# Kernel tuning notes

Hardware: AMD Instinct MI355X
Metric: run time of the kernel (lower is better)

## Reference

```python
import jax, jax.numpy as jnp
import numpy as np
from jax.scipy.special import logsumexp

NEG = -1e9  # surrogate for -inf (keeps masking arithmetic and grads NaN-free)
ABSTRACT_PEN = 0.5


def setup_inputs() -> dict:
    key = jax.random.key(0)
    ks = jax.random.split(key, 5)
    B, T, b = 32, 256, 16
    action_logps = jax.nn.log_softmax(jax.random.normal(ks[0], (B, T, b)), axis=-1)
    stop_logps = jax.nn.log_softmax(jax.random.normal(ks[1], (B, T + 1, b, 2)), axis=-1)
    start_logps = jax.nn.log_softmax(jax.random.normal(ks[2], (B, T + 1, b)), axis=-1)
    causal_pens = jax.random.uniform(ks[3], (B, T + 1, T + 1, b))
    lengths = jax.random.randint(ks[4], (B,), 1, T + 1)
    masks = (jnp.arange(T)[None, :] < lengths[:, None]).astype(jnp.float32)
    return {"action_logps": action_logps, "stop_logps": stop_logps,
            "start_logps": start_logps, "causal_pens": causal_pens,
            "masks": masks, "lengths": lengths}


def _cc_loss(action_logps, stop_logps, start_logps, causal_pens, masks, lengths):
    B, T, b = action_logps.shape
    start_logps = start_logps - ABSTRACT_PEN
    stop_logps = stop_logps[..., ::-1]  # STOP_IX == 0 -> flip so index 1 = stop

    a_ts = jnp.swapaxes(action_logps, 0, 1)            # [T,B,b]
    stop_ts = jnp.swapaxes(stop_logps[:, 1:], 0, 1)    # [T,B,b,2]  stop_logps[:, t+1]
    start_ts = jnp.swapaxes(start_logps[:, :T], 0, 1)  # [T,B,b]
    m_ts = jnp.swapaxes(masks, 0, 1)                   # [T,B]

    # ---- cc_fw: f[t] has shape [B,b,t,2]; pad segment-start axis to T ----
    f0 = jnp.full((B, b, T, 2), NEG).at[:, 0, 0, 1].set(0.0)

    def fw_step(f_prev, xs):
        a_t, stop_t, start_t, t = xs
        # continue current option: positions < t-1
        cont = f_prev[..., 0:1] + a_t[:, :, None, None] + stop_t[:, :, None, :]
        # start a new option at position t-1
        seg = logsumexp(f_prev[..., 1], axis=(1, 2))  # [B]
        new_seg = seg[:, None, None] + start_t[:, :, None] + a_t[:, :, None] + stop_t  # [B,b,2]
        idx = jnp.arange(T)[None, None, :, None]
        f_t = jnp.where(idx == t - 1, new_seg[:, :, None, :], cont)
        return f_t, f_t

    _, F = jax.lax.scan(fw_step, f0, (a_ts, stop_ts, start_ts, jnp.arange(1, T + 1)))
    F_full = jnp.concatenate([f0[None], F], axis=0)  # [T+1,B,b,T,2]
    total_logp = logsumexp(F_full[lengths, jnp.arange(B)][..., 1], axis=(1, 2))  # [B]

    # ---- cc_bw ----
    fT = jnp.full((B, b, 2), NEG).at[:, :, 1].set(0.0)

    def bw_step(f_next, xs):
        a_t, stop_t, start_t, m_t = xs
        f0c = a_t + logsumexp(stop_t + f_next, axis=2)  # [B,b]
        f1c = logsumexp(start_t[:, :, None] + a_t[:, :, None] + stop_t + f_next, axis=(1, 2))  # [B]
        f_t = jnp.stack([f0c, jnp.broadcast_to(f1c[:, None], f0c.shape)], axis=-1)
        done = jnp.stack([jnp.full_like(f0c, NEG), jnp.zeros_like(f0c)], axis=-1)
        f_t = jnp.where(m_t[:, None, None] > 0, f_t, done)
        return f_t, f_t

    _, BW = jax.lax.scan(bw_step, fT, (a_ts, stop_ts, start_ts, m_ts), reverse=True)
    BW_full = jnp.concatenate([BW, fT[None]], axis=0)  # [T+1,B,b,2]

    # ---- causal-consistency penalty expectation ----
    # marginal[t-1, B, b, start] = fw f[t][...,1] + bw f[t][...,1]
    marg = F[..., 1] + BW_full[1:][..., 1][:, :, :, None]          # [T,B,b,T]
    probs = jnp.exp(marg - total_logp[None, :, None, None])        # padded starts -> 0
    # pen[t-1, B, b, start] = causal_pens[B, start, t, b]
    pen = jnp.transpose(causal_pens[:, :T, 1:, :], (2, 0, 3, 1))   # [T,B,b,T]
    total_cc = jnp.sum(jnp.sum(probs * pen, axis=(2, 3)) * m_ts)
    return jnp.stack([jnp.sum(total_logp), total_cc])


def reference(action_logps, stop_logps, start_logps, causal_pens, masks, lengths):
    return _cc_loss(action_logps, stop_logps, start_logps, causal_pens, masks, lengths)
```

## Files before the change

kernel.cpp:

```cpp
#include <hip/hip_runtime.h>

constexpr int B  = 32;
constexpr int T  = 256;
constexpr int NB = 16;
#define NEGV   (-1000000000.0f)
#define INVLN2 1.4426950408889634f
#define LN2    0.6931471805599453f
#define AP2    (0.5f * 1.4426950408889634f)

__device__ __forceinline__ float fexp2(float x) { return exp2f(x); }
__device__ __forceinline__ float flog2(float x) { return __log2f(x); }

template<int C>
__device__ __forceinline__ float dppmv(float x) {
    return __int_as_float(__builtin_amdgcn_update_dpp(
        0, __float_as_int(x), C, 0xF, 0xF, true));
}

__device__ __forceinline__ float lse16_2(float y) {
    float m = y;
    m = fmaxf(m, dppmv<0xB1>(m));
    m = fmaxf(m, dppmv<0x4E>(m));
    m = fmaxf(m, dppmv<0x141>(m));
    m = fmaxf(m, dppmv<0x140>(m));
    float s = fexp2(y - m);
    s += dppmv<0xB1>(s);
    s += dppmv<0x4E>(s);
    s += dppmv<0x141>(s);
    s += dppmv<0x140>(s);
    return m + flog2(s);
}

__device__ __forceinline__ float lse2_2(float a, float b) {
    float m = fmaxf(a, b);
    return m + flog2(fexp2(a - m) + fexp2(b - m));
}

__global__ __launch_bounds__(256) void scan_kernel(
    const float* __restrict__ act_g,
    const float* __restrict__ stp_g,
    const float* __restrict__ str_g,
    const int*   __restrict__ len_g,
    float* __restrict__ Wbuf,
    float* __restrict__ TLbuf,
    float* __restrict__ Ubuf,
    float* __restrict__ Vbuf)
{
    __shared__ float sm[16384];
    float* act  = sm;
    float* stp  = sm + 4096;
    float* strt = sm + 4096 + 8192;

    const int beta = blockIdx.x;
    const int tid  = threadIdx.x;

    {
        const float4* a4 = (const float4*)(act_g + (size_t)beta * (T * NB));
        const float4* s4 = (const float4*)(stp_g + (size_t)beta * ((T + 1) * NB * 2) + 32);
        const float4* t4 = (const float4*)(str_g + (size_t)beta * ((T + 1) * NB));
        float4* actv = (float4*)act;
        float4* stpv = (float4*)stp;
        float4* strv = (float4*)strt;
        for (int i = tid; i < 1024; i += 256) {
            float4 v = a4[i];
            actv[i] = make_float4(v.x*INVLN2, v.y*INVLN2, v.z*INVLN2, v.w*INVLN2);
        }
        for (int i = tid; i < 2048; i += 256) {
            float4 v = s4[i];
            stpv[i] = make_float4(v.x*INVLN2, v.y*INVLN2, v.z*INVLN2, v.w*INVLN2);
        }
        for (int i = tid; i < 1024; i += 256) {
            float4 v = t4[i];
            strv[i] = make_float4(v.x*INVLN2, v.y*INVLN2, v.z*INVLN2, v.w*INVLN2);
        }
    }
    __syncthreads();

    const int wid  = tid >> 6;
    const int lane = tid & 63;
    const int b    = lane & 15;
    const int L    = len_g[beta];

    if (wid == 0) {
        float* Ub = Ubuf + (size_t)beta * (T * NB);
        float* Vb = Vbuf + (size_t)beta * ((T + 1) * NB);
        float PA = 0.f, Q = 0.f;
        float R = strt[b] - AP2;
        if (lane < 16) Ub[b] = R;
        float TL = 0.f;

        float  ca  = act[b];
        float2 cs  = *(const float2*)(stp + b * 2);
        float  cst = strt[16 + b];

        for (int t = 1; t <= T; ++t) {
            float  na  = act[(t & 255) * 16 + b];
            float2 ns  = *(const float2*)(stp + (t & 255) * 32 + b * 2);
            float  nst = strt[((t + 1) & 255) * 16 + b];

            PA += ca;
            float V = PA + Q + cs.x;
            float G = lse16_2(R + V);
            if (t == L) TL = G;
            Q += cs.y;
            if (lane < 16) Vb[t * 16 + b] = V;
            if (t < T) {
                float U = G + (cst - AP2) - PA - Q;
                if (lane < 16) Ub[t * 16 + b] = U;
                R = lse2_2(R, U);
            }
            ca = na; cs = ns; cst = nst;
        }
        if (lane == 0) TLbuf[beta] = TL;
    } else if (wid == 1) {
        float fn0 = NEGV, fn1 = 0.f;
        if (lane == 0) Wbuf[beta * (T + 1) + T] = 0.f;

        float  ca  = act[(T - 1) * 16 + b];
        float2 cs  = *(const float2*)(stp + (T - 1) * 32 + b * 2);
        float  cst = strt[(T - 1) * 16 + b];

        for (int i = T - 1; i >= 0; --i) {
            const int pr = (i - 1) & 255;
            float  na  = act[pr * 16 + b];
            float2 ns  = *(const float2*)(stp + pr * 32 + b * 2);
            float  nst = strt[pr * 16 + b];

            float t0  = cs.y + fn0;
            float t1  = cs.x + fn1;
            float f0c = ca + lse2_2(t0, t1);
            float f1c = lse16_2((cst - AP2) + f0c);
            const bool mk = (i < L);
            fn0 = mk ? f0c : NEGV;
            fn1 = mk ? f1c : 0.f;
            if (i >= 1 && lane == 0) Wbuf[beta * (T + 1) + i] = fn1;
            ca = na; cs = ns; cst = nst;
        }
    }
}

__global__ __launch_bounds__(256) void cc_kernel(
    const float* __restrict__ pens,
    const int*   __restrict__ len_g,
    const float* __restrict__ Wbuf,
    const float* __restrict__ TLbuf,
    const float* __restrict__ Ubuf,
    const float* __restrict__ Vbuf,
    float* __restrict__ part)
{
    const int beta = blockIdx.x;
    const int t    = blockIdx.y + 1;
    const int tid  = threadIdx.x;
    const int pidx = blockIdx.y * B + beta;
    const int L    = len_g[beta];
    if (t > L) { if (tid == 0) part[pidx] = 0.f; return; }

    const float c0 = Wbuf[beta * (T + 1) + t] - TLbuf[beta];
    const float4* U4 = (const float4*)(Ubuf + (size_t)beta * (T * NB));
    const float4* P4 = (const float4*)(pens + (size_t)beta * ((size_t)(T+1)*(T+1)*NB)
                                            + (size_t)t * NB);
    const int q = tid & 3;
    float4 vq = ((const float4*)(Vbuf + (size_t)beta * ((T + 1) * NB) + t * NB))[q];
    vq.x += c0; vq.y += c0; vq.z += c0; vq.w += c0;

    float local = 0.f;
    const int n4 = t * 4;
    for (int i4 = tid; i4 < n4; i4 += 256) {
        const int tau = i4 >> 2;
        float4 u = U4[i4];
        float4 p = P4[(size_t)tau * ((T + 1) * 4) + (i4 & 3)];
        local += fexp2(u.x + vq.x) * p.x + fexp2(u.y + vq.y) * p.y
               + fexp2(u.z + vq.z) * p.z + fexp2(u.w + vq.w) * p.w;
    }
#pragma unroll
    for (int off = 1; off < 64; off <<= 1) local += __shfl_xor(local, off);
    __shared__ float red[4];
    if ((tid & 63) == 0) red[tid >> 6] = local;
    __syncthreads();
    if (tid == 0) part[pidx] = red[0] + red[1] + red[2] + red[3];
}

__global__ __launch_bounds__(256) void final_kernel(
    const float* __restrict__ part, const float* __restrict__ TLbuf,
    float* __restrict__ out)
{
    const int tid = threadIdx.x;
    const float4* p4 = (const float4*)part;
    float s = 0.f;
#pragma unroll
    for (int k = 0; k < 8; ++k) {
        float4 v = p4[tid + 256 * k];
        s += v.x + v.y + v.z + v.w;
    }
#pragma unroll
    for (int off = 1; off < 64; off <<= 1) s += __shfl_xor(s, off);
    __shared__ float red[4];
    if ((tid & 63) == 0) red[tid >> 6] = s;
    __syncthreads();
    if (tid == 0) out[1] = red[0] + red[1] + red[2] + red[3];

    float tl = (tid < 32) ? TLbuf[tid] : 0.f;
    if (tid < 64) {
#pragma unroll
        for (int off = 1; off < 32; off <<= 1) tl += __shfl_xor(tl, off);
        if (tid == 0) out[0] = tl * LN2;
    }
}

extern "C" void kernel_launch(void* const* d_in, const int* in_sizes, int n_in,
                              void* d_out, int out_size, void* d_ws, size_t ws_size,
                              hipStream_t stream) {
    (void)in_sizes; (void)n_in; (void)out_size; (void)ws_size;
    const float* act  = (const float*)d_in[0];
    const float* stp  = (const float*)d_in[1];
    const float* strt = (const float*)d_in[2];
    const float* pens = (const float*)d_in[3];
    const int*   lens = (const int*)d_in[5];
    float* out = (float*)d_out;

    float* ws    = (float*)d_ws;
    float* Wbuf  = ws;
    float* TLbuf = Wbuf + B * (T + 1);
    float* Ubuf  = TLbuf + B;
    float* Vbuf  = Ubuf + (size_t)B * T * NB;
    float* part  = Vbuf + (size_t)B * (T+1) * NB;

    scan_kernel<<<B, 256, 0, stream>>>(act, stp, strt, lens, Wbuf, TLbuf, Ubuf, Vbuf);
    cc_kernel<<<dim3(B, T), 256, 0, stream>>>(pens, lens, Wbuf, TLbuf, Ubuf, Vbuf, part);
    final_kernel<<<1, 256, 0, stream>>>(part, TLbuf, out);
}
```

Before: 258.6 us.

## Replace log-space scan recurrences with scaled linear-space recurrences

The forward and backward serial scans now carry their state in linear probability space and rescale it by a power of two taken from the exponent bits, with the running exponent kept in a separate accumulator. This replaces the per-step max reductions, the logsumexp pairs and most exp/log calls with multiply-adds and one 16-lane sum. The aim is to shorten the latency-bound serial dependency chain of the scan kernel. The cost is reliance on the scaling to avoid underflow or overflow in float32, which could reduce accuracy for extreme inputs.

```diff
diff --git a/kernel.cpp b/kernel.cpp
--- a/kernel.cpp
+++ b/kernel.cpp
@@ -3,7 +3,6 @@
 constexpr int B  = 32;
 constexpr int T  = 256;
 constexpr int NB = 16;
-#define NEGV   (-1000000000.0f)
 #define INVLN2 1.4426950408889634f
 #define LN2    0.6931471805599453f
 #define AP2    (0.5f * 1.4426950408889634f)
@@ -17,23 +16,12 @@
         0, __float_as_int(x), C, 0xF, 0xF, true));
 }
 
-__device__ __forceinline__ float lse16_2(float y) {
-    float m = y;
-    m = fmaxf(m, dppmv<0xB1>(m));
-    m = fmaxf(m, dppmv<0x4E>(m));
-    m = fmaxf(m, dppmv<0x141>(m));
-    m = fmaxf(m, dppmv<0x140>(m));
-    float s = fexp2(y - m);
-    s += dppmv<0xB1>(s);
-    s += dppmv<0x4E>(s);
-    s += dppmv<0x141>(s);
-    s += dppmv<0x140>(s);
-    return m + flog2(s);
-}
-
-__device__ __forceinline__ float lse2_2(float a, float b) {
-    float m = fmaxf(a, b);
-    return m + flog2(fexp2(a - m) + fexp2(b - m));
+__device__ __forceinline__ float sum16(float x) {
+    x += dppmv<0xB1>(x);
+    x += dppmv<0x4E>(x);
+    x += dppmv<0x141>(x);
+    x += dppmv<0x140>(x);
+    return x;
 }
 
 __global__ __launch_bounds__(256) void scan_kernel(
@@ -84,10 +72,10 @@
     if (wid == 0) {
         float* Ub = Ubuf + (size_t)beta * (T * NB);
         float* Vb = Vbuf + (size_t)beta * ((T + 1) * NB);
-        float PA = 0.f, Q = 0.f;
-        float R = strt[b] - AP2;
-        if (lane < 16) Ub[b] = R;
-        float TL = 0.f;
+        float PA = 0.f, Q = 0.f, Z = 0.f, TL = 0.f;
+        float u0 = strt[b] - AP2;
+        float E  = fexp2(u0);
+        if (lane < 16) Ub[b] = u0;
 
         float  ca  = act[b];
         float2 cs  = *(const float2*)(stp + b * 2);
@@ -98,22 +86,29 @@
             float2 ns  = *(const float2*)(stp + (t & 255) * 32 + b * 2);
             float  nst = strt[((t + 1) & 255) * 16 + b];
 
-            PA += ca;
-            float V = PA + Q + cs.x;
-            float G = lse16_2(R + V);
+            float AP0 = fexp2(ca + cs.x);
+            float S   = sum16(E * AP0);
+            float G   = flog2(S) + Z;
             if (t == L) TL = G;
-            Q += cs.y;
+            float V   = PA + ca + Q + cs.x;
+            PA += ca; Q += cs.y;
             if (lane < 16) Vb[t * 16 + b] = V;
             if (t < T) {
-                float U = G + (cst - AP2) - PA - Q;
+                float AP1 = fexp2(ca + cs.y);
+                float Tb  = fexp2(cst - AP2);
+                float U   = G + (cst - AP2) - PA - Q;
                 if (lane < 16) Ub[t * 16 + b] = U;
-                R = lse2_2(R, U);
+                float En  = E * AP1 + S * Tb;
+                unsigned e = (__float_as_uint(S) >> 23) & 0xFFu;
+                float    r = __uint_as_float((254u - e) << 23);
+                E = En * r;
+                Z += (float)((int)e - 127);
             }
             ca = na; cs = ns; cst = nst;
         }
         if (lane == 0) TLbuf[beta] = TL;
     } else if (wid == 1) {
-        float fn0 = NEGV, fn1 = 0.f;
+        float F0 = 0.f, F1 = 1.f, Z = 0.f;
         if (lane == 0) Wbuf[beta * (T + 1) + T] = 0.f;
 
         float  ca  = act[(T - 1) * 16 + b];
@@ -126,14 +121,19 @@
             float2 ns  = *(const float2*)(stp + pr * 32 + b * 2);
             float  nst = strt[pr * 16 + b];
 
-            float t0  = cs.y + fn0;
-            float t1  = cs.x + fn1;
-            float f0c = ca + lse2_2(t0, t1);
-            float f1c = lse16_2((cst - AP2) + f0c);
+            float AP1 = fexp2(ca + cs.y);
+            float AP0 = fexp2(ca + cs.x);
+            float Tb  = fexp2(cst - AP2);
+            float F0n = AP1 * F0 + AP0 * F1;
+            float F1n = sum16(Tb * F0n);
             const bool mk = (i < L);
-            fn0 = mk ? f0c : NEGV;
-            fn1 = mk ? f1c : 0.f;
-            if (i >= 1 && lane == 0) Wbuf[beta * (T + 1) + i] = fn1;
+            float W = flog2(F1n) + Z;
+            unsigned e = (__float_as_uint(F1n) >> 23) & 0xFFu;
+            float    r = __uint_as_float((254u - e) << 23);
+            F0 = mk ? F0n * r : 0.f;
+            F1 = mk ? F1n * r : 1.f;
+            Z  = mk ? Z + (float)((int)e - 127) : 0.f;
+            if (i >= 1 && lane == 0) Wbuf[beta * (T + 1) + i] = mk ? W : 0.f;
             ca = na; cs = ns; cst = nst;
         }
     }
```

Result: no change. 261.6 us (+1.2%).
